# Optimization experiments

Hardware: AMD Instinct MI355X
Metric: run time of the kernel (lower is better)

The kernel has to match this reference:

```python
import jax, jax.numpy as jnp
import numpy as np

BATCH = 4096
D_IN = 8192
D_OUT = 8192
B = 128            # block size
K_IN = D_IN // B   # 64 (D_IN divisible by B -> no padding)
K_OUT = D_OUT // B # 64 (D_OUT divisible by B -> no trailing slice)
INIT_SCALE = 0.1


def setup_inputs() -> dict:
    key = jax.random.key(0)
    kx, kw, kd = jax.random.split(key, 3)
    x = jax.random.normal(kx, (BATCH, D_IN), dtype=jnp.float32)
    W = jax.random.normal(kw, (K_OUT, K_IN, B), dtype=jnp.float32) * INIT_SCALE
    # Bernoulli +/-1 diagonal signs over input dims
    D = jnp.where(jax.random.bernoulli(kd, p=0.5, shape=(D_IN,)), 1.0, -1.0).astype(jnp.float32)
    return {"x": x, "W": W, "D": D}


def reference(x, W, D):
    # x: (batch, d_in); W: (k_out, k_in, b) first rows of circulant blocks; D: (d_in,) signs
    batch = x.shape[0]
    k_out, k_in, b = W.shape
    x_blocks = (x * D[None, :]).reshape(batch, k_in, b)  # d_in divisible by b -> no pad
    # Batched FFT of all input blocks and all weight first-rows at once
    Xf = jnp.fft.fft(x_blocks, axis=-1)          # (batch, k_in, b) complex
    Wf = jnp.conj(jnp.fft.fft(W, axis=-1))       # (k_out, k_in, b) complex
    # Sum over k_in in the frequency domain: per-frequency complex contraction
    Yf = jnp.einsum('bji,oji->boi', Xf, Wf)      # (batch, k_out, b)
    out = jnp.fft.ifft(Yf, axis=-1).real         # (batch, k_out, b)
    return out.reshape(batch, k_out * b)         # k_out*b == d_out -> no slice
```

## Files before the change

### kernel.cpp

```cpp
#include <hip/hip_runtime.h>


typedef __bf16 bf16;
typedef __bf16 bf16x8 __attribute__((ext_vector_type(8)));
typedef float f32x4 __attribute__((ext_vector_type(4)));

#define PI_F 3.14159265358979323846f

#define WS_B1   0u
#define WS_B2T  49152u
#define WS_WMAT 90112u
#define WS_X    2220032u

__device__ __forceinline__ unsigned int pack_bf2(float a, float b) {
    unsigned short ra = __builtin_bit_cast(unsigned short, (bf16)a);
    unsigned short rb = __builtin_bit_cast(unsigned short, (bf16)b);
    return (unsigned int)ra | ((unsigned int)rb << 16);
}

__global__ __launch_bounds__(256) void init_basis(bf16* __restrict__ B1,
                                                  bf16* __restrict__ B2T) {
    int gid = blockIdx.x * 256 + threadIdx.x;
    if (gid < 192 * 128) {
        int fc = gid >> 7, t = gid & 127;
        int f = fc >> 1;
        float v = 0.f;
        if (f <= 64) {
            int a = (f * t) & 127;
            float ang = a * (PI_F / 64.f);
            v = (fc & 1) ? -__sinf(ang) : __cosf(ang);
        }
        B1[gid] = (bf16)v;
    }
    if (gid < 128 * 160) {
        int t = gid / 160, fc = gid % 160;
        int f = fc >> 1, c = fc & 1;
        float v = 0.f;
        if (f == 0) {
            v = c ? 0.f : (1.f / 128.f);
        } else if (f == 64) {
            v = c ? 0.f : ((t & 1) ? -1.f / 128.f : 1.f / 128.f);
        } else if (f < 64) {
            int a = (f * t) & 127;
            float ang = a * (PI_F / 64.f);
            v = c ? (-2.f / 128.f) * __sinf(ang) : (2.f / 128.f) * __cosf(ang);
        }
        B2T[gid] = (bf16)v;
    }
}

__global__ __launch_bounds__(256) void init_wmat(const float* __restrict__ W,
                                                 bf16* __restrict__ Wm) {
    __shared__ float ct[128], st[128];
    __shared__ float ws[256][17];
    const int tid = threadIdx.x;
    if (tid < 128) {
        float ang = tid * (PI_F / 64.f);
        ct[tid] = __cosf(ang);
        st[tid] = __sinf(ang);
    }
    const int f = blockIdx.x >> 4;
    const int rb = (blockIdx.x & 15) * 256;
    const float* wbase = W + (size_t)rb * 128;
    float wr = 0.f, wi = 0.f;
    for (int tb = 0; tb < 8; tb++) {
        __syncthreads();
#pragma unroll
        for (int i = 0; i < 4; i++) {
            int v = i * 256 + tid;
            int row = v >> 2, seg = v & 3;
            float4 t = *(const float4*)(wbase + (size_t)row * 128 + tb * 16 + seg * 4);
            ws[row][seg * 4 + 0] = t.x;
            ws[row][seg * 4 + 1] = t.y;
            ws[row][seg * 4 + 2] = t.z;
            ws[row][seg * 4 + 3] = t.w;
        }
        __syncthreads();
#pragma unroll
        for (int u = 0; u < 16; u++) {
            int tau = tb * 16 + u;
            float w = ws[tid][u];
            int a = (f * tau) & 127;
            wr += w * ct[a];
            wi += w * st[a];
        }
    }
    const int row = rb + tid;
    const int o = row >> 6, j = row & 63;
    bf16* base = Wm + ((size_t)f * 128 + 2 * o) * 128 + 2 * j;
    *(unsigned int*)base         = pack_bf2(wr, -wi);
    *(unsigned int*)(base + 128) = pack_bf2(wi, wr);
}

__global__ __launch_bounds__(256) void k1_dft(const float* __restrict__ x,
                                              const float* __restrict__ D,
                                              const bf16* __restrict__ B1,
                                              bf16* __restrict__ X) {
    __shared__ bf16 xs[8][16][136];
    const int tid = threadIdx.x;
    const int wave = tid >> 6, lane = tid & 63;
    const int q = lane >> 4, nl = lane & 15;
    const int s_t = blockIdx.x >> 2, jq = blockIdx.x & 3;
    const int s0 = s_t * 16;
    const bool nt2 = (wave == 0);

    bf16x8 bfrag[3][4];
#pragma unroll
    for (int t = 0; t < 2; t++) {
        int nt = wave + 4 * t;
#pragma unroll
        for (int kc = 0; kc < 4; kc++)
            bfrag[t][kc] = *(const bf16x8*)(B1 + (nt * 16 + nl) * 128 + kc * 32 + q * 8);
    }
    if (nt2) {
#pragma unroll
        for (int kc = 0; kc < 4; kc++)
            bfrag[2][kc] = *(const bf16x8*)(B1 + (128 + nl) * 128 + kc * 32 + q * 8);
    }

    for (int grp = 0; grp < 2; grp++) {
        const int jb = jq * 16 + grp * 8;
        __syncthreads();
        {
            const int jl = tid >> 5, ss = (tid >> 1) & 15, th = tid & 1;
            const float* xp = x + (size_t)(s0 + ss) * 8192 + (jb + jl) * 128 + th * 64;
            const float* Dp = D + (jb + jl) * 128 + th * 64;
            bf16* dst = &xs[jl][ss][th * 64];
#pragma unroll
            for (int u = 0; u < 8; u++) {
                float4 a  = *(const float4*)(xp + u * 8);
                float4 b  = *(const float4*)(xp + u * 8 + 4);
                float4 da = *(const float4*)(Dp + u * 8);
                float4 db = *(const float4*)(Dp + u * 8 + 4);
                bf16x8 o;
                o[0] = (bf16)(a.x * da.x); o[1] = (bf16)(a.y * da.y);
                o[2] = (bf16)(a.z * da.z); o[3] = (bf16)(a.w * da.w);
                o[4] = (bf16)(b.x * db.x); o[5] = (bf16)(b.y * db.y);
                o[6] = (bf16)(b.z * db.z); o[7] = (bf16)(b.w * db.w);
                *(bf16x8*)(dst + u * 8) = o;
            }
        }
        __syncthreads();

        f32x4 acc[3][8];
        const f32x4 zero = {0.f, 0.f, 0.f, 0.f};
#pragma unroll
        for (int t = 0; t < 3; t++)
#pragma unroll
            for (int j = 0; j < 8; j++) acc[t][j] = zero;

#pragma unroll
        for (int j = 0; j < 8; j++) {
#pragma unroll
            for (int kc = 0; kc < 4; kc++) {
                bf16x8 a = *(const bf16x8*)&xs[j][nl][kc * 32 + q * 8];
                acc[0][j] = __builtin_amdgcn_mfma_f32_16x16x32_bf16(
                    a, bfrag[0][kc], acc[0][j], 0, 0, 0);
                acc[1][j] = __builtin_amdgcn_mfma_f32_16x16x32_bf16(
                    a, bfrag[1][kc], acc[1][j], 0, 0, 0);
            }
        }
        if (nt2) {
#pragma unroll
            for (int j = 0; j < 8; j++) {
#pragma unroll
                for (int kc = 0; kc < 4; kc++) {
                    bf16x8 a = *(const bf16x8*)&xs[j][nl][kc * 32 + q * 8];
                    acc[2][j] = __builtin_amdgcn_mfma_f32_16x16x32_bf16(
                        a, bfrag[2][kc], acc[2][j], 0, 0, 0);
                }
            }
        }

        const int par = lane & 1;
#pragma unroll
        for (int t = 0; t < 3; t++) {
            if (t == 2 && !nt2) continue;
            const int fc = (wave + 4 * t) * 16 + nl;
            const int fpr = fc >> 1;
            const bool wr = (fc < 130);
#pragma unroll
            for (int r = 0; r < 4; r++) {
                float sh[8];
#pragma unroll
                for (int j = 0; j < 8; j++)
                    sh[j] = __shfl_xor(acc[t][j][r], 1);
                unsigned int d0, d1, d2, d3;
                if (!par) {
                    d0 = pack_bf2(acc[t][0][r], sh[0]);
                    d1 = pack_bf2(acc[t][1][r], sh[1]);
                    d2 = pack_bf2(acc[t][2][r], sh[2]);
                    d3 = pack_bf2(acc[t][3][r], sh[3]);
                } else {
                    d0 = pack_bf2(sh[4], acc[t][4][r]);
                    d1 = pack_bf2(sh[5], acc[t][5][r]);
                    d2 = pack_bf2(sh[6], acc[t][6][r]);
                    d3 = pack_bf2(sh[7], acc[t][7][r]);
                }
                if (wr) {
                    char* p = (char*)X + ((size_t)fpr * 4096 + s0 + q * 4 + r) * 256
                              + jb * 4 + par * 16;
                    *(uint4*)p = make_uint4(d0, d1, d2, d3);
                }
            }
        }
    }
}

__global__ __launch_bounds__(256, 4) void k2_gemm(const bf16* __restrict__ X,
                                                  const bf16* __restrict__ Wmat,
                                                  const bf16* __restrict__ B2T,
                                                  float* __restrict__ out) {
    __shared__ bf16 ybuf[8 * 16 * 136 + 32];
    const int tid = threadIdx.x;
    const int wave = tid >> 6, lane = tid & 63;
    const int q = lane >> 4, nl = lane & 15;
    const int bid = blockIdx.x;
    const int xcd = bid & 7, seq = bid >> 3;
    const int s_t = xcd + 8 * (seq >> 3);
    const int o_t = seq & 7;
    const int s0 = s_t * 16;

    {
        unsigned int* yz = (unsigned int*)ybuf;
        for (int i = tid; i < (8 * 16 * 136 + 32) / 2; i += 256) yz[i] = 0u;
    }

    const bf16* wp = Wmat + (size_t)(o_t * 16 + nl) * 128 + q * 8;
    const bf16* xp = X + (size_t)(s0 + nl) * 128 + q * 8;

    bf16x8 wa[4], xa[4], wb[4], xb[4];
    auto loadf = [&](int f, bf16x8 (&wf)[4], bf16x8 (&xf)[4]) {
#pragma unroll
        for (int kc = 0; kc < 4; kc++) {
            wf[kc] = *(const bf16x8*)(wp + (size_t)f * 16384 + kc * 32);
            xf[kc] = *(const bf16x8*)(xp + (size_t)f * 524288 + kc * 32);
        }
    };
    auto compute = [&](int f, bf16x8 (&wf)[4], bf16x8 (&xf)[4]) {
        f32x4 acc = {0.f, 0.f, 0.f, 0.f};
#pragma unroll
        for (int kc = 0; kc < 4; kc++)
            acc = __builtin_amdgcn_mfma_f32_16x16x32_bf16(wf[kc], xf[kc], acc, 0, 0, 0);
        const int o0 = q * 2, o1 = o0 + 1;
        const int fb = f >> 2, fo = (f & 3) * 2;
        const int b0 = (fb < 16) ? (fb ^ o0) : fb;
        const int b1 = (fb < 16) ? (fb ^ o1) : fb;
        *(unsigned int*)&ybuf[(o0 * 16 + nl) * 136 + b0 * 8 + fo] = pack_bf2(acc[0], acc[1]);
        *(unsigned int*)&ybuf[(o1 * 16 + nl) * 136 + b1 * 8 + fo] = pack_bf2(acc[2], acc[3]);
    };

    loadf(wave, wa, xa);
    __syncthreads();

    for (int g = 0; g < 9; g++) {
        const int f0 = g * 8 + wave;
        const int f1 = f0 + 4;
        const int f2 = f0 + 8;
        if (f1 < 65) loadf(f1, wb, xb);
        if (f0 < 65) compute(f0, wa, xa);
        if (f2 < 65) loadf(f2, wa, xa);
        if (f1 < 65) compute(f1, wb, xb);
    }

    bf16x8 bt[2][5];
#pragma unroll
    for (int h = 0; h < 2; h++) {
        const int nt = wave + 4 * h;
#pragma unroll
        for (int kc = 0; kc < 5; kc++)
            bt[h][kc] = *(const bf16x8*)(B2T + (nt * 16 + nl) * 160 + kc * 32 + q * 8);
    }
    __syncthreads();

#pragma unroll
    for (int o = 0; o < 8; o++) {
#pragma unroll
        for (int h = 0; h < 2; h++) {
            f32x4 acc = {0.f, 0.f, 0.f, 0.f};
#pragma unroll
            for (int kc = 0; kc < 5; kc++) {
                const int bb = kc * 4 + q;
                const int bs = (bb < 16) ? (bb ^ o) : bb;
                bf16x8 a = *(const bf16x8*)&ybuf[(o * 16 + nl) * 136 + bs * 8];
                acc = __builtin_amdgcn_mfma_f32_16x16x32_bf16(a, bt[h][kc], acc, 0, 0, 0);
            }
            const int nt = wave + 4 * h;
            float* op = out + (size_t)(s0 + q * 4) * 8192 + (o_t * 8 + o) * 128 + nt * 16 + nl;
#pragma unroll
            for (int r = 0; r < 4; r++)
                op[(size_t)r * 8192] = acc[r];
        }
    }
}

extern "C" void kernel_launch(void* const* d_in, const int* in_sizes, int n_in,
                              void* d_out, int out_size, void* d_ws, size_t ws_size,
                              hipStream_t stream) {
    const float* x = (const float*)d_in[0];
    const float* W = (const float*)d_in[1];
    const float* D = (const float*)d_in[2];
    float* out = (float*)d_out;
    char* ws = (char*)d_ws;
    bf16* B1  = (bf16*)(ws + WS_B1);
    bf16* B2T = (bf16*)(ws + WS_B2T);
    bf16* Wm  = (bf16*)(ws + WS_WMAT);
    bf16* X   = (bf16*)(ws + WS_X);

    hipLaunchKernelGGL(init_basis, dim3(96), dim3(256), 0, stream, B1, B2T);
    hipLaunchKernelGGL(init_wmat, dim3(1040), dim3(256), 0, stream, W, Wm);
    hipLaunchKernelGGL(k1_dft, dim3(1024), dim3(256), 0, stream, x, D, B1, X);
    hipLaunchKernelGGL(k2_gemm, dim3(2048), dim3(256), 0, stream, X, Wm, B2T, out);
}
```

Baseline: 410.1 us.

## Stage X tiles through LDS with async global_load_lds double buffering

The frequency-domain GEMM now streams X tiles from global memory straight into a double-buffered, XOR-swizzled LDS stage using global_load_lds. The loop is software-pipelined with explicit vmcnt waits and barriers, and W fragments are still prefetched into registers one step ahead. The aim is to overlap X fetch latency with MFMA work and to cut the vector registers spent on X prefetch. In exchange it uses more LDS and lowers the occupancy hint from 4 to 2 blocks per CU, and the per-step barriers can serialise the waves. The inverse-transform tile assignment also changes to wave*2+h.

```diff
diff --git a/kernel.cpp b/kernel.cpp
--- a/kernel.cpp
+++ b/kernel.cpp
@@ -11,6 +11,10 @@
 #define WS_B2T  49152u
 #define WS_WMAT 90112u
 #define WS_X    2220032u
+
+#define GLOAD_LDS16(g, l) __builtin_amdgcn_global_load_lds( \
+    (const __attribute__((address_space(1))) unsigned int*)(g), \
+    (__attribute__((address_space(3))) unsigned int*)(l), 16, 0, 0)
 
 __device__ __forceinline__ unsigned int pack_bf2(float a, float b) {
     unsigned short ra = __builtin_bit_cast(unsigned short, (bf16)a);
@@ -207,11 +211,12 @@
     }
 }
 
-__global__ __launch_bounds__(256, 4) void k2_gemm(const bf16* __restrict__ X,
+__global__ __launch_bounds__(256, 2) void k2_gemm(const bf16* __restrict__ X,
                                                   const bf16* __restrict__ Wmat,
                                                   const bf16* __restrict__ B2T,
                                                   float* __restrict__ out) {
-    __shared__ bf16 ybuf[8 * 16 * 136 + 32];
+    __shared__ __align__(16) bf16 ybuf[8 * 16 * 136 + 32];
+    __shared__ __align__(16) bf16 xstage[2][4][2048];
     const int tid = threadIdx.x;
     const int wave = tid >> 6, lane = tid & 63;
     const int q = lane >> 4, nl = lane & 15;
@@ -225,48 +230,81 @@
         unsigned int* yz = (unsigned int*)ybuf;
         for (int i = tid; i < (8 * 16 * 136 + 32) / 2; i += 256) yz[i] = 0u;
     }
-
+    __syncthreads();
+
+    int soff[4];
+#pragma unroll
+    for (int r = 0; r < 4; r++) {
+        int s_loc = r * 4 + (lane >> 4);
+        int cg = (lane & 15) ^ (s_loc & 7);
+        soff[r] = (s0 + s_loc) * 256 + cg * 16;
+    }
+    const char* Xb = (const char*)X;
+
+    auto dmaG = [&](int g) {
+        int f = g * 4 + wave;
+        if (f > 64) f = 64;
+        const char* src = Xb + (size_t)f * 1048576u;
+        char* dst = (char*)&xstage[g & 1][wave][0];
+#pragma unroll
+        for (int r = 0; r < 4; r++)
+            GLOAD_LDS16(src + soff[r], dst + r * 1024);
+    };
     const bf16* wp = Wmat + (size_t)(o_t * 16 + nl) * 128 + q * 8;
-    const bf16* xp = X + (size_t)(s0 + nl) * 128 + q * 8;
-
-    bf16x8 wa[4], xa[4], wb[4], xb[4];
-    auto loadf = [&](int f, bf16x8 (&wf)[4], bf16x8 (&xf)[4]) {
-#pragma unroll
-        for (int kc = 0; kc < 4; kc++) {
+    auto loadWG = [&](int g, bf16x8(&wf)[4]) {
+        int f = g * 4 + wave;
+        if (f > 64) f = 64;
+#pragma unroll
+        for (int kc = 0; kc < 4; kc++)
             wf[kc] = *(const bf16x8*)(wp + (size_t)f * 16384 + kc * 32);
-            xf[kc] = *(const bf16x8*)(xp + (size_t)f * 524288 + kc * 32);
-        }
     };
-    auto compute = [&](int f, bf16x8 (&wf)[4], bf16x8 (&xf)[4]) {
-        f32x4 acc = {0.f, 0.f, 0.f, 0.f};
-#pragma unroll
-        for (int kc = 0; kc < 4; kc++)
-            acc = __builtin_amdgcn_mfma_f32_16x16x32_bf16(wf[kc], xf[kc], acc, 0, 0, 0);
-        const int o0 = q * 2, o1 = o0 + 1;
-        const int fb = f >> 2, fo = (f & 3) * 2;
-        const int b0 = (fb < 16) ? (fb ^ o0) : fb;
-        const int b1 = (fb < 16) ? (fb ^ o1) : fb;
-        *(unsigned int*)&ybuf[(o0 * 16 + nl) * 136 + b0 * 8 + fo] = pack_bf2(acc[0], acc[1]);
-        *(unsigned int*)&ybuf[(o1 * 16 + nl) * 136 + b1 * 8 + fo] = pack_bf2(acc[2], acc[3]);
+    auto comp = [&](int g, const bf16x8(&wf)[4]) {
+        const int f = g * 4 + wave;
+        if (f < 65) {
+            const bf16* stg = &xstage[g & 1][wave][0];
+            f32x4 acc = {0.f, 0.f, 0.f, 0.f};
+#pragma unroll
+            for (int kc = 0; kc < 4; kc++) {
+                const int c = (kc * 4 + q) ^ (nl & 7);
+                bf16x8 b = *(const bf16x8*)(stg + nl * 128 + c * 8);
+                acc = __builtin_amdgcn_mfma_f32_16x16x32_bf16(wf[kc], b, acc, 0, 0, 0);
+            }
+            const int o0 = q * 2, o1 = o0 + 1;
+            const int fb = f >> 2, fo = (f & 3) * 2;
+            const int b0 = (fb < 16) ? (fb ^ o0) : fb;
+            const int b1 = (fb < 16) ? (fb ^ o1) : fb;
+            *(unsigned int*)&ybuf[(o0 * 16 + nl) * 136 + b0 * 8 + fo] = pack_bf2(acc[0], acc[1]);
+            *(unsigned int*)&ybuf[(o1 * 16 + nl) * 136 + b1 * 8 + fo] = pack_bf2(acc[2], acc[3]);
+        }
     };
 
-    loadf(wave, wa, xa);
-    __syncthreads();
-
-    for (int g = 0; g < 9; g++) {
-        const int f0 = g * 8 + wave;
-        const int f1 = f0 + 4;
-        const int f2 = f0 + 8;
-        if (f1 < 65) loadf(f1, wb, xb);
-        if (f0 < 65) compute(f0, wa, xa);
-        if (f2 < 65) loadf(f2, wa, xa);
-        if (f1 < 65) compute(f1, wb, xb);
+    bf16x8 wcur[4], wnxt[4];
+    dmaG(0);
+    loadWG(0, wcur);
+    asm volatile("" ::: "memory");
+    __builtin_amdgcn_sched_barrier(0);
+    for (int g = 0; g < 17; g++) {
+        if (g < 16) {
+            dmaG(g + 1);
+            loadWG(g + 1, wnxt);
+        }
+        __builtin_amdgcn_sched_barrier(0);
+        if (g < 16)
+            asm volatile("s_waitcnt vmcnt(8)" ::: "memory");
+        else
+            asm volatile("s_waitcnt vmcnt(0)" ::: "memory");
+        __builtin_amdgcn_s_barrier();
+        __builtin_amdgcn_sched_barrier(0);
+        comp(g, wcur);
+#pragma unroll
+        for (int kc = 0; kc < 4; kc++) wcur[kc] = wnxt[kc];
+        __builtin_amdgcn_sched_barrier(0);
     }
 
     bf16x8 bt[2][5];
 #pragma unroll
     for (int h = 0; h < 2; h++) {
-        const int nt = wave + 4 * h;
+        const int nt = wave * 2 + h;
 #pragma unroll
         for (int kc = 0; kc < 5; kc++)
             bt[h][kc] = *(const bf16x8*)(B2T + (nt * 16 + nl) * 160 + kc * 32 + q * 8);
@@ -285,7 +323,7 @@
                 bf16x8 a = *(const bf16x8*)&ybuf[(o * 16 + nl) * 136 + bs * 8];
                 acc = __builtin_amdgcn_mfma_f32_16x16x32_bf16(a, bt[h][kc], acc, 0, 0, 0);
             }
-            const int nt = wave + 4 * h;
+            const int nt = wave * 2 + h;
             float* op = out + (size_t)(s0 + q * 4) * 8192 + (o_t * 8 + o) * 128 + nt * 16 + nl;
 #pragma unroll
             for (int r = 0; r < 4; r++)
```

Result: faster. 374.0 us (-8.8%).
